# Kernel tuning notes

Hardware: AMD Instinct MI355X
Metric: run time of the kernel (lower is better)

Reference implementation:

```python
import jax, jax.numpy as jnp
import numpy as np

N = 200000
D_STRUCT = 131
D_SPATIAL = 64
D_OUT = 256


def setup_inputs() -> dict:
    key = jax.random.key(0)
    k1, k2, k3, k4, k5, k6, k7 = jax.random.split(key, 7)
    spatial = jax.random.normal(k1, (N, D_SPATIAL), dtype=jnp.float32)
    structural = jax.random.normal(k2, (N, D_STRUCT), dtype=jnp.float32)
    neighbour = jax.random.randint(k3, (N, 3), 0, N, dtype=jnp.int64)
    # Conv1d(kernel=1) params: weight [out_ch, in_ch], bias [out_ch]
    fan_agg = D_STRUCT
    W_agg = jax.random.uniform(k4, (D_OUT, D_STRUCT), dtype=jnp.float32,
                               minval=-1.0, maxval=1.0) / np.sqrt(fan_agg)
    b_agg = jax.random.uniform(k5, (D_OUT,), dtype=jnp.float32,
                               minval=-1.0, maxval=1.0) / np.sqrt(fan_agg)
    fan_comb = D_SPATIAL + D_STRUCT
    W_comb = jax.random.uniform(k6, (D_OUT, D_SPATIAL + D_STRUCT), dtype=jnp.float32,
                                minval=-1.0, maxval=1.0) / np.sqrt(fan_comb)
    b_comb = jax.random.uniform(k7, (D_OUT,), dtype=jnp.float32,
                                minval=-1.0, maxval=1.0) / np.sqrt(fan_comb)
    return {"spatial": spatial, "structural": structural, "neighbour": neighbour,
            "W_agg": W_agg, "b_agg": b_agg, "W_comb": W_comb, "b_comb": b_comb}


def reference(spatial, structural, neighbour, W_agg, b_agg, W_comb, b_comb):
    # Combination1: concat(spatial, structural) -> 1x1 conv (linear)
    a1 = jnp.concatenate([spatial, structural], axis=1)  # [n, 195]
    out1 = a1 @ W_comb.T + b_comb                         # [n, 256]

    # Aggregation1: mean of self + 3 gathered neighbour rows, then linear
    neigh_feats = structural[neighbour]                   # [n, 3, 131]
    agg = (structural + neigh_feats.sum(axis=1)) * 0.25   # [n, 131]
    out2 = agg @ W_agg.T + b_agg                          # [n, 256]
    return (out1, out2)
```

## Files before the change

kernel.cpp:

```cpp
#include <hip/hip_runtime.h>
#include <hip/hip_bf16.h>

#define NROWS   200000
#define DSP     64
#define DST     131
#define DOUT    256
#define K1PAD   224
#define K2PAD   160
#define NK1     7
#define NK2     5
#define BM      64
#define NBLK    (NROWS / BM)
#define LD1     (K1PAD + 8)
#define LD2     (K2PAD + 8)

typedef short bf8   __attribute__((ext_vector_type(8)));
typedef float f32x4 __attribute__((ext_vector_type(4)));
typedef float f4v   __attribute__((ext_vector_type(4)));

__device__ __forceinline__ unsigned short f2bf(float x) {
    unsigned u = __float_as_uint(x);
    unsigned r = (u + 0x7fffu + ((u >> 16) & 1u)) >> 16;
    return (unsigned short)r;
}

__device__ __forceinline__ unsigned short bf1(float x) {
    __hip_bfloat16 h = __float2bfloat16(x);
    return *reinterpret_cast<unsigned short*>(&h);
}
__device__ __forceinline__ unsigned packbf2(float a, float b) {
    return (unsigned)bf1(a) | ((unsigned)bf1(b) << 16);
}

__global__ __launch_bounds__(256) void wprep(const float* __restrict__ Wc,
                                             const float* __restrict__ Wa,
                                             short* __restrict__ w1p,
                                             short* __restrict__ w2p) {
    int idx = blockIdx.x * 256 + threadIdx.x;
    if (idx < 57344) {
        int j  = idx & 7;
        int l  = (idx >> 3) & 63;
        int cb = (idx >> 9) & 15;
        int ks = idx >> 13;
        int k  = ks * 32 + (l >> 4) * 8 + j;
        int n  = cb * 16 + (l & 15);
        float v = (k < 195) ? Wc[n * 195 + k] : 0.0f;
        w1p[idx] = (short)f2bf(v);
    } else {
        int id2 = idx - 57344;
        if (id2 < 40960) {
            int j  = id2 & 7;
            int l  = (id2 >> 3) & 63;
            int cb = (id2 >> 9) & 15;
            int ks = id2 >> 13;
            int k  = ks * 32 + (l >> 4) * 8 + j;
            int n  = cb * 16 + (l & 15);
            float v = (k < 131) ? Wa[n * 131 + k] : 0.0f;
            w2p[id2] = (short)f2bf(v);
        }
    }
}

template <int NK, int LDPAD, int MREP>
__device__ __forceinline__ void mfma_tile_and_store(
        const short (*lds)[LDPAD],
        const short* __restrict__ wp,
        const float* __restrict__ bias,
        float* __restrict__ out,
        int r0, int t) {
    const int wave = t >> 6;
    const int l    = t & 63;
    const int lr   = l & 15;
    const int lk   = l >> 4;

    f32x4 acc[MREP][4];
    #pragma unroll
    for (int m = 0; m < MREP; ++m)
        #pragma unroll
        for (int n = 0; n < 4; ++n)
            acc[m][n] = (f32x4){0.f, 0.f, 0.f, 0.f};

    #pragma unroll
    for (int ks = 0; ks < NK; ++ks) {
        bf8 a[MREP], bb[4];
        #pragma unroll
        for (int m = 0; m < MREP; ++m)
            a[m] = *(const bf8*)&lds[m * 16 + lr][ks * 32 + lk * 8];
        #pragma unroll
        for (int n = 0; n < 4; ++n) {
            int cb = wave * 4 + n;
            bb[n] = *(const bf8*)(wp + (((ks * 16 + cb) * 64 + l) << 3));
        }
        #pragma unroll
        for (int m = 0; m < MREP; ++m)
            #pragma unroll
            for (int n = 0; n < 4; ++n)
                acc[m][n] = __builtin_amdgcn_mfma_f32_16x16x32_bf16(
                                a[m], bb[n], acc[m][n], 0, 0, 0);
    }

    #pragma unroll
    for (int n = 0; n < 4; ++n) {
        int col = wave * 64 + n * 16 + lr;
        float bv = bias[col];
        #pragma unroll
        for (int m = 0; m < MREP; ++m) {
            #pragma unroll
            for (int r = 0; r < 4; ++r) {
                int row = m * 16 + lk * 4 + r;
                __builtin_nontemporal_store(
                    acc[m][n][r] + bv,
                    &out[(size_t)(r0 + row) * DOUT + col]);
            }
        }
    }
}

__global__ __launch_bounds__(256, 3) void fused(
        const float* __restrict__ spatial,
        const float* __restrict__ structural,
        const int*   __restrict__ neigh,
        const short* __restrict__ w1p,
        const short* __restrict__ w2p,
        const float* __restrict__ b_comb,
        const float* __restrict__ b_agg,
        float* __restrict__ out1,
        float* __restrict__ out2) {
    __shared__ short lds1[BM][LD1];
    __shared__ short lds2[BM][LD2];
    const int t  = threadIdx.x;
    const int w  = t >> 6;
    const int l  = t & 63;
    const int r0 = blockIdx.x * BM;

    int nv = 0;
    if (l < 48) {
        int lrow = l / 3;
        int lq   = l - lrow * 3;
        nv = neigh[(r0 + w * 16 + lrow) * 3 + lq];
    }

    {
        int row = w * 16 + (l >> 2);
        int k   = l & 3;
        *(uint4*)&lds1[row][192 + 8 * k] = make_uint4(0, 0, 0, 0);
        *(uint4*)&lds2[row][128 + 8 * k] = make_uint4(0, 0, 0, 0);
    }

    {
        int h  = t & 15;
        int sl = t >> 4;
        #pragma unroll
        for (int p = 0; p < 4; ++p) {
            int row = sl + 16 * p;
            f4v v = __builtin_nontemporal_load(
                (const f4v*)(spatial + (size_t)(r0 + row) * DSP + 4 * h));
            uint2 wv;
            wv.x = packbf2(v.x, v.y);
            wv.y = packbf2(v.z, v.w);
            *(uint2*)&lds1[row][4 * h] = wv;
        }
    }

    {
        const char* sbase = (const char*)structural;
        const int h   = l >> 5;
        const int sub = l & 31;
        #pragma unroll
        for (int p = 0; p < 8; ++p) {
            int local = 2 * p + h;
            int row   = w * 16 + local;
            int srow  = r0 + row;
            int n0 = __shfl(nv, 3 * local + 0);
            int n1 = __shfl(nv, 3 * local + 1);
            int n2 = __shfl(nv, 3 * local + 2);

            unsigned co = 16u * (unsigned)sub;
            float4 v0 = *(const float4*)(sbase + (unsigned)srow * 524u + co);
            float4 v1 = *(const float4*)(sbase + (unsigned)n0   * 524u + co);
            float4 v2 = *(const float4*)(sbase + (unsigned)n1   * 524u + co);
            float4 v3 = *(const float4*)(sbase + (unsigned)n2   * 524u + co);

            uint2 wa;
            wa.x = packbf2(v0.x, v0.y);
            wa.y = packbf2(v0.z, v0.w);
            *(uint2*)&lds1[row][64 + 4 * sub] = wa;

            float sx = (v0.x + v1.x + v2.x + v3.x) * 0.25f;
            float sy = (v0.y + v1.y + v2.y + v3.y) * 0.25f;
            float sz = (v0.z + v1.z + v2.z + v3.z) * 0.25f;
            float sw = (v0.w + v1.w + v2.w + v3.w) * 0.25f;
            uint2 wb;
            wb.x = packbf2(sx, sy);
            wb.y = packbf2(sz, sw);
            *(uint2*)&lds2[row][4 * sub] = wb;

            if (sub == 31) {
                unsigned to = 508u;
                float4 t0 = *(const float4*)(sbase + (unsigned)srow * 524u + to);
                float4 t1 = *(const float4*)(sbase + (unsigned)n0   * 524u + to);
                float4 t2 = *(const float4*)(sbase + (unsigned)n1   * 524u + to);
                float4 t3 = *(const float4*)(sbase + (unsigned)n2   * 524u + to);
                *(unsigned*)&lds1[row][192] = packbf2(t0.y, t0.z);
                lds1[row][194] = (short)bf1(t0.w);
                float ty = (t0.y + t1.y + t2.y + t3.y) * 0.25f;
                float tz = (t0.z + t1.z + t2.z + t3.z) * 0.25f;
                float tw = (t0.w + t1.w + t2.w + t3.w) * 0.25f;
                *(unsigned*)&lds2[row][128] = packbf2(ty, tz);
                lds2[row][130] = (short)bf1(tw);
            }
        }
    }
    __syncthreads();

    mfma_tile_and_store<NK1, LD1, BM / 16>(lds1, w1p, b_comb, out1, r0, t);
    mfma_tile_and_store<NK2, LD2, BM / 16>(lds2, w2p, b_agg, out2, r0, t);
}

extern "C" void kernel_launch(void* const* d_in, const int* in_sizes, int n_in,
                              void* d_out, int out_size, void* d_ws, size_t ws_size,
                              hipStream_t stream) {
    const float* spatial    = (const float*)d_in[0];
    const float* structural = (const float*)d_in[1];
    const int*   neighbour  = (const int*)  d_in[2];
    const float* W_agg      = (const float*)d_in[3];
    const float* b_agg      = (const float*)d_in[4];
    const float* W_comb     = (const float*)d_in[5];
    const float* b_comb     = (const float*)d_in[6];

    float* out1 = (float*)d_out;
    float* out2 = out1 + (size_t)NROWS * DOUT;

    short* w1p = (short*)d_ws;
    short* w2p = w1p + 57344;

    wprep<<<384, 256, 0, stream>>>(W_comb, W_agg, w1p, w2p);
    fused<<<NBLK, 256, 0, stream>>>(spatial, structural, neighbour,
                                    w1p, w2p, b_comb, b_agg, out1, out2);
}
```

Measured before the change: 173.7 us.

## Pre-convert structural features to padded bf16 rows before neighbour gather

```diff
diff --git a/kernel.cpp b/kernel.cpp
--- a/kernel.cpp
+++ b/kernel.cpp
@@ -4,6 +4,7 @@
 #define NROWS   200000
 #define DSP     64
 #define DST     131
+#define DSTP    136
 #define DOUT    256
 #define K1PAD   224
 #define K2PAD   160
@@ -30,6 +31,21 @@
 }
 __device__ __forceinline__ unsigned packbf2(float a, float b) {
     return (unsigned)bf1(a) | ((unsigned)bf1(b) << 16);
+}
+__device__ __forceinline__ float blo(unsigned u) { return __uint_as_float(u << 16); }
+__device__ __forceinline__ float bhi(unsigned u) { return __uint_as_float(u & 0xffff0000u); }
+
+__device__ __forceinline__ uint4 agg4(uint4 a, uint4 b, uint4 c, uint4 d) {
+    uint4 r;
+    #pragma unroll
+    for (int i = 0; i < 4; ++i) {
+        unsigned ua = (&a.x)[i], ub = (&b.x)[i];
+        unsigned uc = (&c.x)[i], ud = (&d.x)[i];
+        float lo = (blo(ua) + blo(ub)) + (blo(uc) + blo(ud));
+        float hi = (bhi(ua) + bhi(ub)) + (bhi(uc) + bhi(ud));
+        (&r.x)[i] = packbf2(lo * 0.25f, hi * 0.25f);
+    }
+    return r;
 }
 
 __global__ __launch_bounds__(256) void wprep(const float* __restrict__ Wc,
@@ -61,6 +77,33 @@
     }
 }
 
+__global__ __launch_bounds__(256) void cvt(const float* __restrict__ st,
+                                           unsigned short* __restrict__ sbf) {
+    int wid = (blockIdx.x * 256 + threadIdx.x) >> 6;
+    int l   = threadIdx.x & 63;
+    int h   = l >> 5, sub = l & 31;
+    int nw  = (gridDim.x * 256) >> 6;
+    for (int pr = wid; pr < NROWS / 2; pr += nw) {
+        int row = pr * 2 + h;
+        const float* src = st + (size_t)row * DST;
+        unsigned short* dst = sbf + (size_t)row * DSTP;
+        f4v v = __builtin_nontemporal_load((const f4v*)(src + 4 * sub));
+        uint2 wv;
+        wv.x = packbf2(v.x, v.y);
+        wv.y = packbf2(v.z, v.w);
+        *(uint2*)(dst + 4 * sub) = wv;
+        if (sub == 0) {
+            float4 tl = *(const float4*)(src + 127);
+            uint4 tw;
+            tw.x = packbf2(tl.y, tl.z);
+            tw.y = packbf2(tl.w, 0.0f);
+            tw.z = 0u;
+            tw.w = 0u;
+            *(uint4*)(dst + 128) = tw;
+        }
+    }
+}
+
 template <int NK, int LDPAD, int MREP>
 __device__ __forceinline__ void mfma_tile_and_store(
         const short (*lds)[LDPAD],
@@ -118,7 +161,7 @@
 
 __global__ __launch_bounds__(256, 3) void fused(
         const float* __restrict__ spatial,
-        const float* __restrict__ structural,
+        const unsigned short* __restrict__ sbf,
         const int*   __restrict__ neigh,
         const short* __restrict__ w1p,
         const short* __restrict__ w2p,
@@ -137,7 +180,8 @@
     if (l < 48) {
         int lrow = l / 3;
         int lq   = l - lrow * 3;
-        nv = neigh[(r0 + w * 16 + lrow) * 3 + lq];
+        nv = __builtin_nontemporal_load(
+                 neigh + (r0 + w * 16 + lrow) * 3 + lq);
     }
 
     {
@@ -163,52 +207,38 @@
     }
 
     {
-        const char* sbase = (const char*)structural;
-        const int h   = l >> 5;
-        const int sub = l & 31;
-        #pragma unroll
-        for (int p = 0; p < 8; ++p) {
-            int local = 2 * p + h;
+        const char* sb = (const char*)sbf;
+        const int c  = l & 15;
+        const int rp = l >> 4;
+        const unsigned co = 16u * (unsigned)c;
+        #pragma unroll
+        for (int p = 0; p < 4; ++p) {
+            int local = p * 4 + rp;
             int row   = w * 16 + local;
             int srow  = r0 + row;
             int n0 = __shfl(nv, 3 * local + 0);
             int n1 = __shfl(nv, 3 * local + 1);
             int n2 = __shfl(nv, 3 * local + 2);
-
-            unsigned co = 16u * (unsigned)sub;
-            float4 v0 = *(const float4*)(sbase + (unsigned)srow * 524u + co);
-            float4 v1 = *(const float4*)(sbase + (unsigned)n0   * 524u + co);
-            float4 v2 = *(const float4*)(sbase + (unsigned)n1   * 524u + co);
-            float4 v3 = *(const float4*)(sbase + (unsigned)n2   * 524u + co);
-
-            uint2 wa;
-            wa.x = packbf2(v0.x, v0.y);
-            wa.y = packbf2(v0.z, v0.w);
-            *(uint2*)&lds1[row][64 + 4 * sub] = wa;
-
-            float sx = (v0.x + v1.x + v2.x + v3.x) * 0.25f;
-            float sy = (v0.y + v1.y + v2.y + v3.y) * 0.25f;
-            float sz = (v0.z + v1.z + v2.z + v3.z) * 0.25f;
-            float sw = (v0.w + v1.w + v2.w + v3.w) * 0.25f;
-            uint2 wb;
-            wb.x = packbf2(sx, sy);
-            wb.y = packbf2(sz, sw);
-            *(uint2*)&lds2[row][4 * sub] = wb;
-
-            if (sub == 31) {
-                unsigned to = 508u;
-                float4 t0 = *(const float4*)(sbase + (unsigned)srow * 524u + to);
-                float4 t1 = *(const float4*)(sbase + (unsigned)n0   * 524u + to);
-                float4 t2 = *(const float4*)(sbase + (unsigned)n1   * 524u + to);
-                float4 t3 = *(const float4*)(sbase + (unsigned)n2   * 524u + to);
-                *(unsigned*)&lds1[row][192] = packbf2(t0.y, t0.z);
-                lds1[row][194] = (short)bf1(t0.w);
-                float ty = (t0.y + t1.y + t2.y + t3.y) * 0.25f;
-                float tz = (t0.z + t1.z + t2.z + t3.z) * 0.25f;
-                float tw = (t0.w + t1.w + t2.w + t3.w) * 0.25f;
-                *(unsigned*)&lds2[row][128] = packbf2(ty, tz);
-                lds2[row][130] = (short)bf1(tw);
-            }
+            uint4 s0 = *(const uint4*)(sb + (unsigned)srow * 272u + co);
+            uint4 s1 = *(const uint4*)(sb + (unsigned)n0   * 272u + co);
+            uint4 s2 = *(const uint4*)(sb + (unsigned)n1   * 272u + co);
+            uint4 s3 = *(const uint4*)(sb + (unsigned)n2   * 272u + co);
+            *(uint4*)&lds1[row][64 + 8 * c] = s0;
+            *(uint4*)&lds2[row][8 * c]      = agg4(s0, s1, s2, s3);
+        }
+        int tl_ = l & 15;
+        int ti0 = __shfl(nv, 3 * tl_ + 0);
+        int ti1 = __shfl(nv, 3 * tl_ + 1);
+        int ti2 = __shfl(nv, 3 * tl_ + 2);
+        if (l < 16) {
+            int row  = w * 16 + l;
+            int srow = r0 + row;
+            uint4 s0 = *(const uint4*)(sb + (unsigned)srow * 272u + 256u);
+            uint4 s1 = *(const uint4*)(sb + (unsigned)ti0  * 272u + 256u);
+            uint4 s2 = *(const uint4*)(sb + (unsigned)ti1  * 272u + 256u);
+            uint4 s3 = *(const uint4*)(sb + (unsigned)ti2  * 272u + 256u);
+            *(uint4*)&lds1[row][192] = s0;
+            *(uint4*)&lds2[row][128] = agg4(s0, s1, s2, s3);
         }
     }
     __syncthreads();
@@ -233,8 +263,10 @@
 
     short* w1p = (short*)d_ws;
     short* w2p = w1p + 57344;
+    unsigned short* sbf = (unsigned short*)((char*)d_ws + 196608);
 
     wprep<<<384, 256, 0, stream>>>(W_comb, W_agg, w1p, w2p);
-    fused<<<NBLK, 256, 0, stream>>>(spatial, structural, neighbour,
+    cvt<<<2048, 256, 0, stream>>>(structural, sbf);
+    fused<<<NBLK, 256, 0, stream>>>(spatial, sbf, neighbour,
                                     w1p, w2p, b_comb, b_agg, out1, out2);
 }
```

Result: slower. 177.9 us (+2.4%).

## Alias LDS buffers and split kernel into two sequential phases for occupancy

Applied to the files above, without the earlier changes.

```diff
diff --git a/kernel.cpp b/kernel.cpp
--- a/kernel.cpp
+++ b/kernel.cpp
@@ -116,7 +116,7 @@
     }
 }
 
-__global__ __launch_bounds__(256, 3) void fused(
+__global__ __launch_bounds__(256, 5) void fused(
         const float* __restrict__ spatial,
         const float* __restrict__ structural,
         const int*   __restrict__ neigh,
@@ -127,26 +127,26 @@
         float* __restrict__ out1,
         float* __restrict__ out2) {
     __shared__ short lds1[BM][LD1];
-    __shared__ short lds2[BM][LD2];
+    short (*lds2)[LD2] = (short (*)[LD2])&lds1[0][0];
     const int t  = threadIdx.x;
     const int w  = t >> 6;
     const int l  = t & 63;
     const int r0 = blockIdx.x * BM;
+    const char* sbase = (const char*)structural;
 
     int nv = 0;
     if (l < 48) {
         int lrow = l / 3;
         int lq   = l - lrow * 3;
-        nv = neigh[(r0 + w * 16 + lrow) * 3 + lq];
+        nv = __builtin_nontemporal_load(
+                 neigh + (r0 + w * 16 + lrow) * 3 + lq);
     }
 
     {
         int row = w * 16 + (l >> 2);
         int k   = l & 3;
         *(uint4*)&lds1[row][192 + 8 * k] = make_uint4(0, 0, 0, 0);
-        *(uint4*)&lds2[row][128 + 8 * k] = make_uint4(0, 0, 0, 0);
-    }
-
+    }
     {
         int h  = t & 15;
         int sl = t >> 4;
@@ -161,11 +161,43 @@
             *(uint2*)&lds1[row][4 * h] = wv;
         }
     }
-
-    {
-        const char* sbase = (const char*)structural;
+    {
         const int h   = l >> 5;
         const int sub = l & 31;
+        const unsigned co = 16u * (unsigned)sub;
+        #pragma unroll
+        for (int p = 0; p < 8; ++p) {
+            int row  = w * 16 + 2 * p + h;
+            int srow = r0 + row;
+            float4 v0 = *(const float4*)(sbase + (unsigned)srow * 524u + co);
+            uint2 wa;
+            wa.x = packbf2(v0.x, v0.y);
+            wa.y = packbf2(v0.z, v0.w);
+            *(uint2*)&lds1[row][64 + 4 * sub] = wa;
+        }
+        if (l < 48) {
+            int lrow = l / 3;
+            int q    = l - 3 * lrow;
+            int row  = w * 16 + lrow;
+            int srow = r0 + row;
+            float s0 = *(const float*)(sbase + (unsigned)srow * 524u
+                                              + (unsigned)(128 + q) * 4u);
+            lds1[row][192 + q] = (short)bf1(s0);
+        }
+    }
+    __syncthreads();
+    mfma_tile_and_store<NK1, LD1, BM / 16>(lds1, w1p, b_comb, out1, r0, t);
+    __syncthreads();
+
+    {
+        int row = w * 16 + (l >> 2);
+        int k   = l & 3;
+        *(uint4*)&lds2[row][128 + 8 * k] = make_uint4(0, 0, 0, 0);
+    }
+    {
+        const int h   = l >> 5;
+        const int sub = l & 31;
+        const unsigned co = 16u * (unsigned)sub;
         #pragma unroll
         for (int p = 0; p < 8; ++p) {
             int local = 2 * p + h;
@@ -174,18 +206,10 @@
             int n0 = __shfl(nv, 3 * local + 0);
             int n1 = __shfl(nv, 3 * local + 1);
             int n2 = __shfl(nv, 3 * local + 2);
-
-            unsigned co = 16u * (unsigned)sub;
             float4 v0 = *(const float4*)(sbase + (unsigned)srow * 524u + co);
             float4 v1 = *(const float4*)(sbase + (unsigned)n0   * 524u + co);
             float4 v2 = *(const float4*)(sbase + (unsigned)n1   * 524u + co);
             float4 v3 = *(const float4*)(sbase + (unsigned)n2   * 524u + co);
-
-            uint2 wa;
-            wa.x = packbf2(v0.x, v0.y);
-            wa.y = packbf2(v0.z, v0.w);
-            *(uint2*)&lds1[row][64 + 4 * sub] = wa;
-
             float sx = (v0.x + v1.x + v2.x + v3.x) * 0.25f;
             float sy = (v0.y + v1.y + v2.y + v3.y) * 0.25f;
             float sz = (v0.z + v1.z + v2.z + v3.z) * 0.25f;
@@ -194,26 +218,24 @@
             wb.x = packbf2(sx, sy);
             wb.y = packbf2(sz, sw);
             *(uint2*)&lds2[row][4 * sub] = wb;
-
-            if (sub == 31) {
-                unsigned to = 508u;
-                float4 t0 = *(const float4*)(sbase + (unsigned)srow * 524u + to);
-                float4 t1 = *(const float4*)(sbase + (unsigned)n0   * 524u + to);
-                float4 t2 = *(const float4*)(sbase + (unsigned)n1   * 524u + to);
-                float4 t3 = *(const float4*)(sbase + (unsigned)n2   * 524u + to);
-                *(unsigned*)&lds1[row][192] = packbf2(t0.y, t0.z);
-                lds1[row][194] = (short)bf1(t0.w);
-                float ty = (t0.y + t1.y + t2.y + t3.y) * 0.25f;
-                float tz = (t0.z + t1.z + t2.z + t3.z) * 0.25f;
-                float tw = (t0.w + t1.w + t2.w + t3.w) * 0.25f;
-                *(unsigned*)&lds2[row][128] = packbf2(ty, tz);
-                lds2[row][130] = (short)bf1(tw);
-            }
+        }
+        if (l < 48) {
+            int lrow = l / 3;
+            int q    = l - 3 * lrow;
+            int row  = w * 16 + lrow;
+            int srow = r0 + row;
+            int i0 = __shfl(nv, 3 * lrow + 0);
+            int i1 = __shfl(nv, 3 * lrow + 1);
+            int i2 = __shfl(nv, 3 * lrow + 2);
+            unsigned off = (unsigned)(128 + q) * 4u;
+            float s0 = *(const float*)(sbase + (unsigned)srow * 524u + off);
+            float s1 = *(const float*)(sbase + (unsigned)i0   * 524u + off);
+            float s2 = *(const float*)(sbase + (unsigned)i1   * 524u + off);
+            float s3 = *(const float*)(sbase + (unsigned)i2   * 524u + off);
+            lds2[row][128 + q] = (short)bf1((s0 + s1 + s2 + s3) * 0.25f);
         }
     }
     __syncthreads();
-
-    mfma_tile_and_store<NK1, LD1, BM / 16>(lds1, w1p, b_comb, out1, r0, t);
     mfma_tile_and_store<NK2, LD2, BM / 16>(lds2, w2p, b_agg, out2, r0, t);
 }
 
```

Result: slower. 349.0 us (+100.9%).
